# Kernel tuning notes

Measured on AMD Instinct MI355X. Metric: run time of the kernel, lower is better.

Reference implementation:

```python
import jax, jax.numpy as jnp
import numpy as np

CHEBY = 3  # max_degree / number of Chebyshev polynomial orders
IN_F, OUT_F = 64, 64
B, N = 32, 2048


def setup_inputs() -> dict:
    key = jax.random.key(0)
    k1, k2, k3, k4, k5 = jax.random.split(key, 5)
    stdv = 1.0 / np.sqrt(OUT_F)
    stdv2 = 1.0  # 1/sqrt(K.size(1)) = 1/sqrt(1)
    x = jax.random.normal(k1, (B, N, IN_F), dtype=jnp.float32)
    adj = jax.random.uniform(k2, (B, N, N), dtype=jnp.float32)
    weight = jax.random.uniform(k3, (IN_F, OUT_F), minval=-stdv, maxval=stdv, dtype=jnp.float32)
    K = jax.random.uniform(k4, (CHEBY, 1), minval=-stdv2, maxval=stdv2, dtype=jnp.float32)
    bias = jax.random.uniform(k5, (OUT_F,), minval=-stdv, maxval=stdv, dtype=jnp.float32)
    return {"x": x, "adj": adj, "weight": weight, "K": K, "bias": bias}


def chebyshev_stack(x, adj, max_degree):
    # T_0 = x, T_1 = A x, T_k = 2 A T_{k-1} - T_{k-2}; stack along new last axis
    Ts = [x]
    if max_degree > 1:
        Ts.append(jnp.einsum('bnm,bmf->bnf', adj, x))
    for _ in range(2, max_degree):
        Ts.append(2.0 * jnp.einsum('bnm,bmf->bnf', adj, Ts[-1]) - Ts[-2])
    return jnp.stack(Ts, axis=-1)  # [B, N, F, K]


def reference(x, adj, weight, K, bias):
    support = chebyshev_stack(x, adj, CHEBY)            # [B, N, F, K]
    combined = jnp.einsum('bnfk,ko->bnf', support, K)   # K-weighted sum -> [B, N, F]
    out = jnp.einsum('bnf,fo->bno', combined, weight) + bias
    return out
```

## Files before the change

kernel.cpp:

```cpp
#include <hip/hip_runtime.h>
#include <stdint.h>

#define NN 2048
#define FF 64
#define NB 32

typedef __attribute__((ext_vector_type(8))) short bf16x8;
typedef __attribute__((ext_vector_type(4))) float f32x4;

__device__ __forceinline__ uint16_t f2bf(float f) {
  uint32_t u = __builtin_bit_cast(uint32_t, f);
  return (uint16_t)((u + 0x7FFFu + ((u >> 16) & 1u)) >> 16);
}
__device__ __forceinline__ float bf2f(uint16_t h) {
  uint32_t u = ((uint32_t)h) << 16;
  return __builtin_bit_cast(float, u);
}

__global__ void k_prep(const float* __restrict__ W, uint16_t* __restrict__ Wt) {
  int t = threadIdx.x;
  for (int i = 0; i < 16; ++i) {
    int idx = t * 16 + i;
    int k = idx >> 6, f = idx & 63;
    Wt[f * 64 + k] = f2bf(W[idx]);
  }
}

__global__ __launch_bounds__(256) void k_xw(const float* __restrict__ x,
                                            const uint16_t* __restrict__ Wt,
                                            uint16_t* __restrict__ xw) {
  __shared__ short As[64 * 72];
  int bid = blockIdx.x;
  int b = bid >> 5;
  int n0 = (bid & 31) * 64;
  int t = threadIdx.x;
  const float* xb = x + ((size_t)b * NN + n0) * FF;
  for (int i = 0; i < 4; ++i) {
    int idx = t + i * 256;
    int r = idx >> 4, c = (idx & 15) * 4;
    float4 v = *(const float4*)(xb + r * FF + c);
    uint32_t p0 = f2bf(v.x) | ((uint32_t)f2bf(v.y) << 16);
    uint32_t p1 = f2bf(v.z) | ((uint32_t)f2bf(v.w) << 16);
    uint2 pv = {p0, p1};
    *(uint2*)&As[r * 72 + c] = pv;
  }
  __syncthreads();
  int lane = t & 63, wave = t >> 6;
  int l16 = lane & 15, quad = lane >> 4;
  f32x4 acc[4] = {};
  for (int ks = 0; ks < 2; ++ks) {
    bf16x8 a = *(const bf16x8*)&As[(wave * 16 + l16) * 72 + ks * 32 + quad * 8];
    for (int fi = 0; fi < 4; ++fi) {
      bf16x8 bq = *(const bf16x8*)(Wt + (fi * 16 + l16) * 64 + ks * 32 + quad * 8);
      acc[fi] = __builtin_amdgcn_mfma_f32_16x16x32_bf16(a, bq, acc[fi], 0, 0, 0);
    }
  }
  for (int fi = 0; fi < 4; ++fi)
    for (int r = 0; r < 4; ++r) {
      int n = n0 + wave * 16 + quad * 4 + r;
      int f = fi * 16 + l16;
      xw[((size_t)b * NN + n) * FF + f] = f2bf(acc[fi][r]);
    }
}

__global__ __launch_bounds__(256) void k_tr(const uint16_t* __restrict__ src,
                                            uint16_t* __restrict__ dst) {
  __shared__ uint16_t T[64 * 72];
  int bid = blockIdx.x;
  int b = bid >> 5;
  int n0 = (bid & 31) * 64;
  int t = threadIdx.x;
  for (int j = 0; j < 2; ++j) {
    int n = (t >> 3) + j * 32;
    int f8 = (t & 7) * 8;
    uint4 v = *(const uint4*)(src + ((size_t)b * NN + n0 + n) * FF + f8);
    *(uint4*)&T[n * 72 + f8] = v;
  }
  __syncthreads();
  for (int j = 0; j < 2; ++j) {
    int f = (t >> 3) + j * 32;
    int n8 = (t & 7) * 8;
    uint4 v;
    uint16_t* tp = (uint16_t*)&v;
    for (int i = 0; i < 8; ++i) tp[i] = T[(n8 + i) * 72 + f];
    *(uint4*)(dst + ((size_t)b * FF + f) * NN + n0 + n8) = v;
  }
}

template <int EPI>
__global__ __launch_bounds__(256) void k_gemm(const float* __restrict__ adj,
                                              const uint16_t* __restrict__ Bt,
                                              uint16_t* __restrict__ Yb,
                                              const uint16_t* __restrict__ xw,
                                              const uint16_t* __restrict__ y1,
                                              const float* __restrict__ Kc,
                                              const float* __restrict__ bias,
                                              float* __restrict__ out) {
  __shared__ short As[128 * 72];
  __shared__ short Bs[64 * 72];
  int bid = blockIdx.x;
  int b = bid & 31;
  int rt = bid >> 5;
  int row0 = rt * 128;
  int koff = (((b * 11) + rt * 7) & 31) << 6;
  int t = threadIdx.x;
  const float* Ab = adj + (size_t)b * NN * NN + (size_t)row0 * NN;
  const uint16_t* Btb = Bt + (size_t)b * FF * NN;

  int ar = t >> 4, ac4 = (t & 15) * 4;
  int bfb = t >> 3, bc8 = (t & 7) * 8;

  float4 areg[8];
  uint4 breg[2];
  for (int i = 0; i < 8; ++i)
    areg[i] = *(const float4*)(Ab + (size_t)(ar + i * 16) * NN + koff + ac4);
  for (int j = 0; j < 2; ++j)
    breg[j] = *(const uint4*)(Btb + (size_t)(bfb + j * 32) * NN + koff + bc8);

  f32x4 acc[2][4] = {};
  int lane = t & 63, wave = t >> 6;
  int l16 = lane & 15, quad = lane >> 4;

  for (int it = 0; it < 32; ++it) {
    __syncthreads();
    for (int i = 0; i < 8; ++i) {
      float4 v = areg[i];
      uint32_t p0 = f2bf(v.x) | ((uint32_t)f2bf(v.y) << 16);
      uint32_t p1 = f2bf(v.z) | ((uint32_t)f2bf(v.w) << 16);
      uint2 pv = {p0, p1};
      *(uint2*)&As[(ar + i * 16) * 72 + ac4] = pv;
    }
    for (int j = 0; j < 2; ++j)
      *(uint4*)&Bs[(bfb + j * 32) * 72 + bc8] = breg[j];
    __syncthreads();
    if (it + 1 < 32) {
      int kn = ((it + 1) * 64 + koff) & (NN - 1);
      for (int i = 0; i < 8; ++i)
        areg[i] = *(const float4*)(Ab + (size_t)(ar + i * 16) * NN + kn + ac4);
      for (int j = 0; j < 2; ++j)
        breg[j] = *(const uint4*)(Btb + (size_t)(bfb + j * 32) * NN + kn + bc8);
    }
    for (int ks = 0; ks < 2; ++ks) {
      bf16x8 af[2];
      for (int mi = 0; mi < 2; ++mi)
        af[mi] = *(const bf16x8*)&As[(wave * 32 + mi * 16 + l16) * 72 + ks * 32 + quad * 8];
      for (int fi = 0; fi < 4; ++fi) {
        bf16x8 bq = *(const bf16x8*)&Bs[(fi * 16 + l16) * 72 + ks * 32 + quad * 8];
        acc[0][fi] = __builtin_amdgcn_mfma_f32_16x16x32_bf16(af[0], bq, acc[0][fi], 0, 0, 0);
        acc[1][fi] = __builtin_amdgcn_mfma_f32_16x16x32_bf16(af[1], bq, acc[1][fi], 0, 0, 0);
      }
    }
  }

  if (EPI == 0) {
    for (int mi = 0; mi < 2; ++mi)
      for (int fi = 0; fi < 4; ++fi)
        for (int r = 0; r < 4; ++r) {
          int n = row0 + wave * 32 + mi * 16 + quad * 4 + r;
          int f = fi * 16 + l16;
          Yb[((size_t)b * NN + n) * FF + f] = f2bf(acc[mi][fi][r]);
        }
  } else {
    float ka = Kc[0] - Kc[2], kb = Kc[1], kc = 2.0f * Kc[2];
    for (int mi = 0; mi < 2; ++mi)
      for (int fi = 0; fi < 4; ++fi) {
        int f = fi * 16 + l16;
        float bv = bias[f];
        for (int r = 0; r < 4; ++r) {
          int n = row0 + wave * 32 + mi * 16 + quad * 4 + r;
          size_t idx = ((size_t)b * NN + n) * FF + f;
          out[idx] = ka * bf2f(xw[idx]) + kb * bf2f(y1[idx]) + kc * acc[mi][fi][r] + bv;
        }
      }
  }
}

extern "C" void kernel_launch(void* const* d_in, const int* in_sizes, int n_in,
                              void* d_out, int out_size, void* d_ws, size_t ws_size,
                              hipStream_t stream) {
  const float* x    = (const float*)d_in[0];
  const float* adj  = (const float*)d_in[1];
  const float* W    = (const float*)d_in[2];
  const float* K    = (const float*)d_in[3];
  const float* bias = (const float*)d_in[4];
  float* out = (float*)d_out;

  uint8_t* ws = (uint8_t*)d_ws;
  const size_t SZ = (size_t)NB * NN * FF * sizeof(uint16_t);
  uint16_t* xw_n = (uint16_t*)(ws);
  uint16_t* xwT  = (uint16_t*)(ws + SZ);
  uint16_t* y1_n = (uint16_t*)(ws + 2 * SZ);
  uint16_t* y1T  = (uint16_t*)(ws + 3 * SZ);
  uint16_t* Wt   = (uint16_t*)(ws + 4 * SZ);

  k_prep<<<dim3(1), dim3(256), 0, stream>>>(W, Wt);
  k_xw<<<dim3(1024), dim3(256), 0, stream>>>(x, Wt, xw_n);
  k_tr<<<dim3(1024), dim3(256), 0, stream>>>(xw_n, xwT);
  k_gemm<0><<<dim3(512), dim3(256), 0, stream>>>(adj, xwT, y1_n, nullptr, nullptr,
                                                 nullptr, nullptr, nullptr);
  k_tr<<<dim3(1024), dim3(256), 0, stream>>>(y1_n, y1T);
  k_gemm<1><<<dim3(512), dim3(256), 0, stream>>>(adj, y1T, nullptr, xw_n, y1_n,
                                                 K, bias, out);
}
```

Baseline: 872.0 us.

## Pre-convert adjacency to swizzled bf16 tiles and stream them into LDS asynchronously

Adds a pass that converts the fp32 adjacency into bf16, stored as pre-swizzled 128x64 tiles in workspace. The B operands are transposed into matching swizzled 64x64 tiles. A new GEMM kernel pulls both tiles straight into double-buffered LDS with global_load_lds, replacing the register-staged fp32 load and per-iteration conversion. This halves the bytes each GEMM reads and moves conversion out of the inner loop, but adds a full conversion pass over the adjacency and needs a large workspace. The old path is kept as a fallback when the workspace is too small.

Measured after the change: 877.2 us. No clear change (+0.6%).

```diff
diff --git a/kernel.cpp b/kernel.cpp
--- a/kernel.cpp
+++ b/kernel.cpp
@@ -15,6 +15,12 @@
 __device__ __forceinline__ float bf2f(uint16_t h) {
   uint32_t u = ((uint32_t)h) << 16;
   return __builtin_bit_cast(float, u);
+}
+
+__device__ __forceinline__ void gll16(const void* g, void* l) {
+  __builtin_amdgcn_global_load_lds(
+      (const __attribute__((address_space(1))) void*)g,
+      (__attribute__((address_space(3))) void*)l, 16, 0, 0);
 }
 
 __global__ void k_prep(const float* __restrict__ W, uint16_t* __restrict__ Wt) {
@@ -63,93 +69,124 @@
     }
 }
 
-__global__ __launch_bounds__(256) void k_tr(const uint16_t* __restrict__ src,
-                                            uint16_t* __restrict__ dst) {
+__global__ __launch_bounds__(256) void k_conv(const float* __restrict__ adj,
+                                              uint16_t* __restrict__ adjb) {
+  int bid = blockIdx.x;
+  int b = bid >> 8, rg = bid & 255;
+  int n0 = rg * 8;
+  int t = threadIdx.x;
+  const float* src = adj + ((size_t)b * NN + n0) * NN;
+  char* dstb = (char*)adjb;
+  for (int i = 0; i < 16; ++i) {
+    int idx = i * 256 + t;
+    int r8 = idx >> 9, f4 = idx & 511;
+    float4 v = *(const float4*)(src + (size_t)r8 * NN + f4 * 4);
+    int n = n0 + r8;
+    int rt = n >> 7, r = n & 127;
+    int col = f4 * 4;
+    int kt = col >> 6, c = col & 63;
+    uint32_t p0 = f2bf(v.x) | ((uint32_t)f2bf(v.y) << 16);
+    uint32_t p1 = f2bf(v.z) | ((uint32_t)f2bf(v.w) << 16);
+    uint2 pv = {p0, p1};
+    size_t tb = ((size_t)((b * 16 + rt) * 32 + kt)) * 16384;
+    int off = (r * 128 + c * 2) ^ ((r & 7) << 4);
+    *(uint2*)(dstb + tb + off) = pv;
+  }
+}
+
+__global__ __launch_bounds__(256) void k_trb(const uint16_t* __restrict__ src,
+                                             uint16_t* __restrict__ dst) {
   __shared__ uint16_t T[64 * 72];
   int bid = blockIdx.x;
-  int b = bid >> 5;
-  int n0 = (bid & 31) * 64;
+  int b = bid >> 5, kt = bid & 31;
   int t = threadIdx.x;
   for (int j = 0; j < 2; ++j) {
-    int n = (t >> 3) + j * 32;
-    int f8 = (t & 7) * 8;
-    uint4 v = *(const uint4*)(src + ((size_t)b * NN + n0 + n) * FF + f8);
+    int idx = j * 256 + t;
+    int n = idx >> 3, f8 = (idx & 7) * 8;
+    uint4 v = *(const uint4*)(src + ((size_t)b * NN + kt * 64 + n) * FF + f8);
     *(uint4*)&T[n * 72 + f8] = v;
   }
   __syncthreads();
+  char* tile = (char*)dst + ((size_t)b * 32 + kt) * 8192;
   for (int j = 0; j < 2; ++j) {
     int f = (t >> 3) + j * 32;
     int n8 = (t & 7) * 8;
     uint4 v;
     uint16_t* tp = (uint16_t*)&v;
     for (int i = 0; i < 8; ++i) tp[i] = T[(n8 + i) * 72 + f];
-    *(uint4*)(dst + ((size_t)b * FF + f) * NN + n0 + n8) = v;
+    int off = (f * 128 + n8 * 2) ^ ((f & 7) << 4);
+    *(uint4*)(tile + off) = v;
   }
 }
 
 template <int EPI>
-__global__ __launch_bounds__(256) void k_gemm(const float* __restrict__ adj,
-                                              const uint16_t* __restrict__ Bt,
-                                              uint16_t* __restrict__ Yb,
-                                              const uint16_t* __restrict__ xw,
-                                              const uint16_t* __restrict__ y1,
-                                              const float* __restrict__ Kc,
-                                              const float* __restrict__ bias,
-                                              float* __restrict__ out) {
-  __shared__ short As[128 * 72];
-  __shared__ short Bs[64 * 72];
+__global__ __launch_bounds__(256) void k_gemmB(const uint16_t* __restrict__ adjb,
+                                               const uint16_t* __restrict__ Bt2,
+                                               uint16_t* __restrict__ Yb,
+                                               const uint16_t* __restrict__ xw,
+                                               const uint16_t* __restrict__ y1,
+                                               const float* __restrict__ Kc,
+                                               const float* __restrict__ bias,
+                                               float* __restrict__ out) {
+  __shared__ short As[2][8192];
+  __shared__ short Bs[2][4096];
   int bid = blockIdx.x;
   int b = bid & 31;
   int rt = bid >> 5;
-  int row0 = rt * 128;
-  int koff = (((b * 11) + rt * 7) & 31) << 6;
-  int t = threadIdx.x;
-  const float* Ab = adj + (size_t)b * NN * NN + (size_t)row0 * NN;
-  const uint16_t* Btb = Bt + (size_t)b * FF * NN;
-
-  int ar = t >> 4, ac4 = (t & 15) * 4;
-  int bfb = t >> 3, bc8 = (t & 7) * 8;
-
-  float4 areg[8];
-  uint4 breg[2];
-  for (int i = 0; i < 8; ++i)
-    areg[i] = *(const float4*)(Ab + (size_t)(ar + i * 16) * NN + koff + ac4);
-  for (int j = 0; j < 2; ++j)
-    breg[j] = *(const uint4*)(Btb + (size_t)(bfb + j * 32) * NN + koff + bc8);
-
-  f32x4 acc[2][4] = {};
+  int row0 = rt << 7;
+  int t = threadIdx.x;
   int lane = t & 63, wave = t >> 6;
   int l16 = lane & 15, quad = lane >> 4;
-
+  int krot = ((b * 11) + rt * 7) & 31;
+
+  const char* Atiles = (const char*)adjb + ((size_t)((b * 16 + rt) * 32)) * 16384;
+  const char* Btiles = (const char*)Bt2 + ((size_t)b * 32) * 8192;
+
+  {
+    const char* at = Atiles + (size_t)krot * 16384;
+    const char* bt = Btiles + (size_t)krot * 8192;
+    for (int i = 0; i < 4; ++i)
+      gll16(at + (wave * 4 + i) * 1024 + lane * 16,
+            (char*)&As[0][0] + (wave * 4 + i) * 1024);
+    for (int i = 0; i < 2; ++i)
+      gll16(bt + (wave * 2 + i) * 1024 + lane * 16,
+            (char*)&Bs[0][0] + (wave * 2 + i) * 1024);
+  }
+
+  f32x4 acc[2][4] = {};
+  int cur = 0;
   for (int it = 0; it < 32; ++it) {
-    __syncthreads();
-    for (int i = 0; i < 8; ++i) {
-      float4 v = areg[i];
-      uint32_t p0 = f2bf(v.x) | ((uint32_t)f2bf(v.y) << 16);
-      uint32_t p1 = f2bf(v.z) | ((uint32_t)f2bf(v.w) << 16);
-      uint2 pv = {p0, p1};
-      *(uint2*)&As[(ar + i * 16) * 72 + ac4] = pv;
-    }
-    for (int j = 0; j < 2; ++j)
-      *(uint4*)&Bs[(bfb + j * 32) * 72 + bc8] = breg[j];
+    asm volatile("s_waitcnt vmcnt(0)" ::: "memory");
     __syncthreads();
     if (it + 1 < 32) {
-      int kn = ((it + 1) * 64 + koff) & (NN - 1);
-      for (int i = 0; i < 8; ++i)
-        areg[i] = *(const float4*)(Ab + (size_t)(ar + i * 16) * NN + kn + ac4);
-      for (int j = 0; j < 2; ++j)
-        breg[j] = *(const uint4*)(Btb + (size_t)(bfb + j * 32) * NN + kn + bc8);
-    }
+      int ktg = (krot + it + 1) & 31;
+      const char* at = Atiles + (size_t)ktg * 16384;
+      const char* bt = Btiles + (size_t)ktg * 8192;
+      for (int i = 0; i < 4; ++i)
+        gll16(at + (wave * 4 + i) * 1024 + lane * 16,
+              (char*)&As[cur ^ 1][0] + (wave * 4 + i) * 1024);
+      for (int i = 0; i < 2; ++i)
+        gll16(bt + (wave * 2 + i) * 1024 + lane * 16,
+              (char*)&Bs[cur ^ 1][0] + (wave * 2 + i) * 1024);
+    }
+    const char* Ab_ = (const char*)&As[cur][0];
+    const char* Bb_ = (const char*)&Bs[cur][0];
     for (int ks = 0; ks < 2; ++ks) {
       bf16x8 af[2];
-      for (int mi = 0; mi < 2; ++mi)
-        af[mi] = *(const bf16x8*)&As[(wave * 32 + mi * 16 + l16) * 72 + ks * 32 + quad * 8];
+      for (int mi = 0; mi < 2; ++mi) {
+        int row = wave * 32 + mi * 16 + l16;
+        int off = (row * 128 + (ks * 32 + quad * 8) * 2) ^ ((row & 7) << 4);
+        af[mi] = *(const bf16x8*)(Ab_ + off);
+      }
       for (int fi = 0; fi < 4; ++fi) {
-        bf16x8 bq = *(const bf16x8*)&Bs[(fi * 16 + l16) * 72 + ks * 32 + quad * 8];
+        int frow = fi * 16 + l16;
+        int boff = (frow * 128 + (ks * 32 + quad * 8) * 2) ^ ((frow & 7) << 4);
+        bf16x8 bq = *(const bf16x8*)(Bb_ + boff);
         acc[0][fi] = __builtin_amdgcn_mfma_f32_16x16x32_bf16(af[0], bq, acc[0][fi], 0, 0, 0);
         acc[1][fi] = __builtin_amdgcn_mfma_f32_16x16x32_bf16(af[1], bq, acc[1][fi], 0, 0, 0);
       }
     }
+    cur ^= 1;
   }
 
   if (EPI == 0) {
@@ -175,6 +212,113 @@
   }
 }
 
+__global__ __launch_bounds__(256) void k_tr(const uint16_t* __restrict__ src,
+                                            uint16_t* __restrict__ dst) {
+  __shared__ uint16_t T[64 * 72];
+  int bid = blockIdx.x;
+  int b = bid >> 5;
+  int n0 = (bid & 31) * 64;
+  int t = threadIdx.x;
+  for (int j = 0; j < 2; ++j) {
+    int n = (t >> 3) + j * 32;
+    int f8 = (t & 7) * 8;
+    uint4 v = *(const uint4*)(src + ((size_t)b * NN + n0 + n) * FF + f8);
+    *(uint4*)&T[n * 72 + f8] = v;
+  }
+  __syncthreads();
+  for (int j = 0; j < 2; ++j) {
+    int f = (t >> 3) + j * 32;
+    int n8 = (t & 7) * 8;
+    uint4 v;
+    uint16_t* tp = (uint16_t*)&v;
+    for (int i = 0; i < 8; ++i) tp[i] = T[(n8 + i) * 72 + f];
+    *(uint4*)(dst + ((size_t)b * FF + f) * NN + n0 + n8) = v;
+  }
+}
+
+template <int EPI>
+__global__ __launch_bounds__(256) void k_gemm(const float* __restrict__ adj,
+                                              const uint16_t* __restrict__ Bt,
+                                              uint16_t* __restrict__ Yb,
+                                              const uint16_t* __restrict__ xw,
+                                              const uint16_t* __restrict__ y1,
+                                              const float* __restrict__ Kc,
+                                              const float* __restrict__ bias,
+                                              float* __restrict__ out) {
+  __shared__ short As[128 * 72];
+  __shared__ short Bs[64 * 72];
+  int bid = blockIdx.x;
+  int b = bid & 31;
+  int rt = bid >> 5;
+  int row0 = rt * 128;
+  int koff = (((b * 11) + rt * 7) & 31) << 6;
+  int t = threadIdx.x;
+  const float* Ab = adj + (size_t)b * NN * NN + (size_t)row0 * NN;
+  const uint16_t* Btb = Bt + (size_t)b * FF * NN;
+  int ar = t >> 4, ac4 = (t & 15) * 4;
+  int bfb = t >> 3, bc8 = (t & 7) * 8;
+  float4 areg[8];
+  uint4 breg[2];
+  for (int i = 0; i < 8; ++i)
+    areg[i] = *(const float4*)(Ab + (size_t)(ar + i * 16) * NN + koff + ac4);
+  for (int j = 0; j < 2; ++j)
+    breg[j] = *(const uint4*)(Btb + (size_t)(bfb + j * 32) * NN + koff + bc8);
+  f32x4 acc[2][4] = {};
+  int lane = t & 63, wave = t >> 6;
+  int l16 = lane & 15, quad = lane >> 4;
+  for (int it = 0; it < 32; ++it) {
+    __syncthreads();
+    for (int i = 0; i < 8; ++i) {
+      float4 v = areg[i];
+      uint32_t p0 = f2bf(v.x) | ((uint32_t)f2bf(v.y) << 16);
+      uint32_t p1 = f2bf(v.z) | ((uint32_t)f2bf(v.w) << 16);
+      uint2 pv = {p0, p1};
+      *(uint2*)&As[(ar + i * 16) * 72 + ac4] = pv;
+    }
+    for (int j = 0; j < 2; ++j)
+      *(uint4*)&Bs[(bfb + j * 32) * 72 + bc8] = breg[j];
+    __syncthreads();
+    if (it + 1 < 32) {
+      int kn = ((it + 1) * 64 + koff) & (NN - 1);
+      for (int i = 0; i < 8; ++i)
+        areg[i] = *(const float4*)(Ab + (size_t)(ar + i * 16) * NN + kn + ac4);
+      for (int j = 0; j < 2; ++j)
+        breg[j] = *(const uint4*)(Btb + (size_t)(bfb + j * 32) * NN + kn + bc8);
+    }
+    for (int ks = 0; ks < 2; ++ks) {
+      bf16x8 af[2];
+      for (int mi = 0; mi < 2; ++mi)
+        af[mi] = *(const bf16x8*)&As[(wave * 32 + mi * 16 + l16) * 72 + ks * 32 + quad * 8];
+      for (int fi = 0; fi < 4; ++fi) {
+        bf16x8 bq = *(const bf16x8*)&Bs[(fi * 16 + l16) * 72 + ks * 32 + quad * 8];
+        acc[0][fi] = __builtin_amdgcn_mfma_f32_16x16x32_bf16(af[0], bq, acc[0][fi], 0, 0, 0);
+        acc[1][fi] = __builtin_amdgcn_mfma_f32_16x16x32_bf16(af[1], bq, acc[1][fi], 0, 0, 0);
+      }
+    }
+  }
+  if (EPI == 0) {
+    for (int mi = 0; mi < 2; ++mi)
+      for (int fi = 0; fi < 4; ++fi)
+        for (int r = 0; r < 4; ++r) {
+          int n = row0 + wave * 32 + mi * 16 + quad * 4 + r;
+          int f = fi * 16 + l16;
+          Yb[((size_t)b * NN + n) * FF + f] = f2bf(acc[mi][fi][r]);
+        }
+  } else {
+    float ka = Kc[0] - Kc[2], kb = Kc[1], kc = 2.0f * Kc[2];
+    for (int mi = 0; mi < 2; ++mi)
+      for (int fi = 0; fi < 4; ++fi) {
+        int f = fi * 16 + l16;
+        float bv = bias[f];
+        for (int r = 0; r < 4; ++r) {
+          int n = row0 + wave * 32 + mi * 16 + quad * 4 + r;
+          size_t idx = ((size_t)b * NN + n) * FF + f;
+          out[idx] = ka * bf2f(xw[idx]) + kb * bf2f(y1[idx]) + kc * acc[mi][fi][r] + bv;
+        }
+      }
+  }
+}
+
 extern "C" void kernel_launch(void* const* d_in, const int* in_sizes, int n_in,
                               void* d_out, int out_size, void* d_ws, size_t ws_size,
                               hipStream_t stream) {
@@ -187,18 +331,31 @@
 
   uint8_t* ws = (uint8_t*)d_ws;
   const size_t SZ = (size_t)NB * NN * FF * sizeof(uint16_t);
+  const size_t ADJB = (size_t)NB * NN * NN * sizeof(uint16_t);
   uint16_t* xw_n = (uint16_t*)(ws);
-  uint16_t* xwT  = (uint16_t*)(ws + SZ);
+  uint16_t* bT0  = (uint16_t*)(ws + SZ);
   uint16_t* y1_n = (uint16_t*)(ws + 2 * SZ);
-  uint16_t* y1T  = (uint16_t*)(ws + 3 * SZ);
+  uint16_t* bT1  = (uint16_t*)(ws + 3 * SZ);
   uint16_t* Wt   = (uint16_t*)(ws + 4 * SZ);
+  uint16_t* adjb = (uint16_t*)(ws + 5 * SZ);
 
   k_prep<<<dim3(1), dim3(256), 0, stream>>>(W, Wt);
   k_xw<<<dim3(1024), dim3(256), 0, stream>>>(x, Wt, xw_n);
-  k_tr<<<dim3(1024), dim3(256), 0, stream>>>(xw_n, xwT);
-  k_gemm<0><<<dim3(512), dim3(256), 0, stream>>>(adj, xwT, y1_n, nullptr, nullptr,
-                                                 nullptr, nullptr, nullptr);
-  k_tr<<<dim3(1024), dim3(256), 0, stream>>>(y1_n, y1T);
-  k_gemm<1><<<dim3(512), dim3(256), 0, stream>>>(adj, y1T, nullptr, xw_n, y1_n,
-                                                 K, bias, out);
-}
+
+  if (ws_size >= 5 * SZ + ADJB) {
+    k_conv<<<dim3(8192), dim3(256), 0, stream>>>(adj, adjb);
+    k_trb<<<dim3(1024), dim3(256), 0, stream>>>(xw_n, bT0);
+    k_gemmB<0><<<dim3(512), dim3(256), 0, stream>>>(adjb, bT0, y1_n, nullptr, nullptr,
+                                                    nullptr, nullptr, nullptr);
+    k_trb<<<dim3(1024), dim3(256), 0, stream>>>(y1_n, bT1);
+    k_gemmB<1><<<dim3(512), dim3(256), 0, stream>>>(adjb, bT1, nullptr, xw_n, y1_n,
+                                                    K, bias, out);
+  } else {
+    k_tr<<<dim3(1024), dim3(256), 0, stream>>>(xw_n, bT0);
+    k_gemm<0><<<dim3(512), dim3(256), 0, stream>>>(adj, bT0, y1_n, nullptr, nullptr,
+                                                   nullptr, nullptr, nullptr);
+    k_tr<<<dim3(1024), dim3(256), 0, stream>>>(y1_n, bT1);
+    k_gemm<1><<<dim3(512), dim3(256), 0, stream>>>(adj, bT1, nullptr, xw_n, y1_n,
+                                                   K, bias, out);
+  }
+}
```

## Fuse transposes into producer epilogues and double-buffer smaller GEMM tiles

Applied to the files above, without the earlier changes.

Removes the standalone transpose kernels by having k_xw and the first GEMM write a transposed bf16 copy through shared memory in their epilogues. Halves the GEMM row tile to 64, doubling the grid, and double-buffers the LDS tiles so each iteration uses one barrier instead of two. Adds a launch-bounds occupancy hint. The aim is to cut extra global traffic and kernel launches and to improve latency hiding while streaming adj. The cost is that each B tile is now reused across fewer rows of adj.

Result: no change. 881.0 us (+1.0%).

```diff
diff --git a/kernel.cpp b/kernel.cpp
--- a/kernel.cpp
+++ b/kernel.cpp
@@ -28,7 +28,8 @@
 
 __global__ __launch_bounds__(256) void k_xw(const float* __restrict__ x,
                                             const uint16_t* __restrict__ Wt,
-                                            uint16_t* __restrict__ xw) {
+                                            uint16_t* __restrict__ xw,
+                                            uint16_t* __restrict__ xwT) {
   __shared__ short As[64 * 72];
   int bid = blockIdx.x;
   int b = bid >> 5;
@@ -61,117 +62,127 @@
       int f = fi * 16 + l16;
       xw[((size_t)b * NN + n) * FF + f] = f2bf(acc[fi][r]);
     }
-}
-
-__global__ __launch_bounds__(256) void k_tr(const uint16_t* __restrict__ src,
-                                            uint16_t* __restrict__ dst) {
-  __shared__ uint16_t T[64 * 72];
-  int bid = blockIdx.x;
-  int b = bid >> 5;
-  int n0 = (bid & 31) * 64;
-  int t = threadIdx.x;
-  for (int j = 0; j < 2; ++j) {
-    int n = (t >> 3) + j * 32;
-    int f8 = (t & 7) * 8;
-    uint4 v = *(const uint4*)(src + ((size_t)b * NN + n0 + n) * FF + f8);
-    *(uint4*)&T[n * 72 + f8] = v;
-  }
   __syncthreads();
-  for (int j = 0; j < 2; ++j) {
-    int f = (t >> 3) + j * 32;
-    int n8 = (t & 7) * 8;
-    uint4 v;
-    uint16_t* tp = (uint16_t*)&v;
-    for (int i = 0; i < 8; ++i) tp[i] = T[(n8 + i) * 72 + f];
-    *(uint4*)(dst + ((size_t)b * FF + f) * NN + n0 + n8) = v;
-  }
+  uint16_t* T = (uint16_t*)As;
+  for (int fi = 0; fi < 4; ++fi)
+    for (int r = 0; r < 4; ++r)
+      T[(fi * 16 + l16) * 72 + wave * 16 + quad * 4 + r] = f2bf(acc[fi][r]);
+  __syncthreads();
+  int f = t >> 2, seg = t & 3;
+  uint4 v0 = *(const uint4*)&T[f * 72 + seg * 16];
+  uint4 v1 = *(const uint4*)&T[f * 72 + seg * 16 + 8];
+  uint16_t* dp = xwT + ((size_t)b * FF + f) * NN + n0 + seg * 16;
+  *(uint4*)dp = v0;
+  *(uint4*)(dp + 8) = v1;
 }
 
 template <int EPI>
-__global__ __launch_bounds__(256) void k_gemm(const float* __restrict__ adj,
-                                              const uint16_t* __restrict__ Bt,
-                                              uint16_t* __restrict__ Yb,
-                                              const uint16_t* __restrict__ xw,
-                                              const uint16_t* __restrict__ y1,
-                                              const float* __restrict__ Kc,
-                                              const float* __restrict__ bias,
-                                              float* __restrict__ out) {
-  __shared__ short As[128 * 72];
-  __shared__ short Bs[64 * 72];
+__global__ __launch_bounds__(256, 4) void k_gemm(const float* __restrict__ adj,
+                                                 const uint16_t* __restrict__ Bt,
+                                                 uint16_t* __restrict__ Yb,
+                                                 uint16_t* __restrict__ YbT,
+                                                 const uint16_t* __restrict__ xw,
+                                                 const uint16_t* __restrict__ y1,
+                                                 const float* __restrict__ Kc,
+                                                 const float* __restrict__ bias,
+                                                 float* __restrict__ out) {
+  __shared__ short As[2][64 * 72];
+  __shared__ short Bs[2][64 * 72];
   int bid = blockIdx.x;
   int b = bid & 31;
   int rt = bid >> 5;
-  int row0 = rt * 128;
-  int koff = (((b * 11) + rt * 7) & 31) << 6;
+  int row0 = rt << 6;
   int t = threadIdx.x;
+  int lane = t & 63, wave = t >> 6;
+  int l16 = lane & 15, quad = lane >> 4;
+  int krot = ((b * 11) + rt * 7) & 31;
   const float* Ab = adj + (size_t)b * NN * NN + (size_t)row0 * NN;
   const uint16_t* Btb = Bt + (size_t)b * FF * NN;
 
-  int ar = t >> 4, ac4 = (t & 15) * 4;
-  int bfb = t >> 3, bc8 = (t & 7) * 8;
-
-  float4 areg[8];
+  int ra[4], ca[4];
+  for (int i = 0; i < 4; ++i) {
+    int chunk = t + i * 256;
+    ra[i] = chunk >> 4;
+    ca[i] = (chunk & 15) * 4;
+  }
+  int fb[2], kb8[2];
+  for (int j = 0; j < 2; ++j) {
+    int chunk = t + j * 256;
+    fb[j] = chunk >> 3;
+    kb8[j] = (chunk & 7) * 8;
+  }
+
+  float4 areg[4];
   uint4 breg[2];
-  for (int i = 0; i < 8; ++i)
-    areg[i] = *(const float4*)(Ab + (size_t)(ar + i * 16) * NN + koff + ac4);
-  for (int j = 0; j < 2; ++j)
-    breg[j] = *(const uint4*)(Btb + (size_t)(bfb + j * 32) * NN + koff + bc8);
-
-  f32x4 acc[2][4] = {};
-  int lane = t & 63, wave = t >> 6;
-  int l16 = lane & 15, quad = lane >> 4;
-
+  {
+    int kn = krot * 64;
+    for (int i = 0; i < 4; ++i)
+      areg[i] = *(const float4*)(Ab + (size_t)ra[i] * NN + kn + ca[i]);
+    for (int j = 0; j < 2; ++j)
+      breg[j] = *(const uint4*)(Btb + (size_t)fb[j] * NN + kn + kb8[j]);
+  }
+
+  f32x4 acc[4] = {};
   for (int it = 0; it < 32; ++it) {
-    __syncthreads();
-    for (int i = 0; i < 8; ++i) {
+    asm volatile("s_waitcnt vmcnt(0)" ::: "memory");
+    int p = it & 1;
+    for (int i = 0; i < 4; ++i) {
       float4 v = areg[i];
       uint32_t p0 = f2bf(v.x) | ((uint32_t)f2bf(v.y) << 16);
       uint32_t p1 = f2bf(v.z) | ((uint32_t)f2bf(v.w) << 16);
       uint2 pv = {p0, p1};
-      *(uint2*)&As[(ar + i * 16) * 72 + ac4] = pv;
+      *(uint2*)&As[p][ra[i] * 72 + ca[i]] = pv;
     }
     for (int j = 0; j < 2; ++j)
-      *(uint4*)&Bs[(bfb + j * 32) * 72 + bc8] = breg[j];
+      *(uint4*)&Bs[p][fb[j] * 72 + kb8[j]] = breg[j];
+    if (it + 1 < 32) {
+      int kn = ((krot + it + 1) & 31) * 64;
+      for (int i = 0; i < 4; ++i)
+        areg[i] = *(const float4*)(Ab + (size_t)ra[i] * NN + kn + ca[i]);
+      for (int j = 0; j < 2; ++j)
+        breg[j] = *(const uint4*)(Btb + (size_t)fb[j] * NN + kn + kb8[j]);
+    }
+    asm volatile("s_waitcnt lgkmcnt(0)" ::: "memory");
+    __builtin_amdgcn_s_barrier();
+    for (int ks = 0; ks < 2; ++ks) {
+      bf16x8 a = *(const bf16x8*)&As[p][(wave * 16 + l16) * 72 + ks * 32 + quad * 8];
+      for (int fi = 0; fi < 4; ++fi) {
+        bf16x8 bq = *(const bf16x8*)&Bs[p][(fi * 16 + l16) * 72 + ks * 32 + quad * 8];
+        acc[fi] = __builtin_amdgcn_mfma_f32_16x16x32_bf16(a, bq, acc[fi], 0, 0, 0);
+      }
+    }
+  }
+
+  if (EPI == 0) {
+    for (int fi = 0; fi < 4; ++fi)
+      for (int r = 0; r < 4; ++r) {
+        int n = row0 + wave * 16 + quad * 4 + r;
+        int f = fi * 16 + l16;
+        Yb[((size_t)b * NN + n) * FF + f] = f2bf(acc[fi][r]);
+      }
     __syncthreads();
-    if (it + 1 < 32) {
-      int kn = ((it + 1) * 64 + koff) & (NN - 1);
-      for (int i = 0; i < 8; ++i)
-        areg[i] = *(const float4*)(Ab + (size_t)(ar + i * 16) * NN + kn + ac4);
-      for (int j = 0; j < 2; ++j)
-        breg[j] = *(const uint4*)(Btb + (size_t)(bfb + j * 32) * NN + kn + bc8);
-    }
-    for (int ks = 0; ks < 2; ++ks) {
-      bf16x8 af[2];
-      for (int mi = 0; mi < 2; ++mi)
-        af[mi] = *(const bf16x8*)&As[(wave * 32 + mi * 16 + l16) * 72 + ks * 32 + quad * 8];
-      for (int fi = 0; fi < 4; ++fi) {
-        bf16x8 bq = *(const bf16x8*)&Bs[(fi * 16 + l16) * 72 + ks * 32 + quad * 8];
-        acc[0][fi] = __builtin_amdgcn_mfma_f32_16x16x32_bf16(af[0], bq, acc[0][fi], 0, 0, 0);
-        acc[1][fi] = __builtin_amdgcn_mfma_f32_16x16x32_bf16(af[1], bq, acc[1][fi], 0, 0, 0);
-      }
-    }
-  }
-
-  if (EPI == 0) {
-    for (int mi = 0; mi < 2; ++mi)
-      for (int fi = 0; fi < 4; ++fi)
-        for (int r = 0; r < 4; ++r) {
-          int n = row0 + wave * 32 + mi * 16 + quad * 4 + r;
-          int f = fi * 16 + l16;
-          Yb[((size_t)b * NN + n) * FF + f] = f2bf(acc[mi][fi][r]);
-        }
+    uint16_t* T = (uint16_t*)&As[0][0];
+    for (int fi = 0; fi < 4; ++fi)
+      for (int r = 0; r < 4; ++r)
+        T[(fi * 16 + l16) * 72 + wave * 16 + quad * 4 + r] = f2bf(acc[fi][r]);
+    __syncthreads();
+    int f = t >> 2, seg = t & 3;
+    uint4 v0 = *(const uint4*)&T[f * 72 + seg * 16];
+    uint4 v1 = *(const uint4*)&T[f * 72 + seg * 16 + 8];
+    uint16_t* dp = YbT + ((size_t)b * FF + f) * NN + row0 + seg * 16;
+    *(uint4*)dp = v0;
+    *(uint4*)(dp + 8) = v1;
   } else {
     float ka = Kc[0] - Kc[2], kb = Kc[1], kc = 2.0f * Kc[2];
-    for (int mi = 0; mi < 2; ++mi)
-      for (int fi = 0; fi < 4; ++fi) {
-        int f = fi * 16 + l16;
-        float bv = bias[f];
-        for (int r = 0; r < 4; ++r) {
-          int n = row0 + wave * 32 + mi * 16 + quad * 4 + r;
-          size_t idx = ((size_t)b * NN + n) * FF + f;
-          out[idx] = ka * bf2f(xw[idx]) + kb * bf2f(y1[idx]) + kc * acc[mi][fi][r] + bv;
-        }
+    for (int fi = 0; fi < 4; ++fi) {
+      int f = fi * 16 + l16;
+      float bv = bias[f];
+      for (int r = 0; r < 4; ++r) {
+        int n = row0 + wave * 16 + quad * 4 + r;
+        size_t idx = ((size_t)b * NN + n) * FF + f;
+        out[idx] = ka * bf2f(xw[idx]) + kb * bf2f(y1[idx]) + kc * acc[fi][r] + bv;
       }
+    }
   }
 }
 
@@ -194,11 +205,9 @@
   uint16_t* Wt   = (uint16_t*)(ws + 4 * SZ);
 
   k_prep<<<dim3(1), dim3(256), 0, stream>>>(W, Wt);
-  k_xw<<<dim3(1024), dim3(256), 0, stream>>>(x, Wt, xw_n);
-  k_tr<<<dim3(1024), dim3(256), 0, stream>>>(xw_n, xwT);
-  k_gemm<0><<<dim3(512), dim3(256), 0, stream>>>(adj, xwT, y1_n, nullptr, nullptr,
-                                                 nullptr, nullptr, nullptr);
-  k_tr<<<dim3(1024), dim3(256), 0, stream>>>(y1_n, y1T);
-  k_gemm<1><<<dim3(512), dim3(256), 0, stream>>>(adj, y1T, nullptr, xw_n, y1_n,
-                                                 K, bias, out);
-}
+  k_xw<<<dim3(1024), dim3(256), 0, stream>>>(x, Wt, xw_n, xwT);
+  k_gemm<0><<<dim3(1024), dim3(256), 0, stream>>>(adj, xwT, y1_n, y1T, nullptr,
+                                                  nullptr, nullptr, nullptr, nullptr);
+  k_gemm<1><<<dim3(1024), dim3(256), 0, stream>>>(adj, y1T, nullptr, nullptr, xw_n,
+                                                  y1_n, K, bias, out);
+}
```
